# Kernel tuning notes

Hardware: AMD Instinct MI355X
Metric: run time of the kernel (lower is better)

## Reference

```python
import jax, jax.numpy as jnp
import numpy as np

N = 65536        # nodes = x_feature_num * batch_size
F_IN = 1024      # x_feature_num (conv1 in_channels)
E = 2097152      # edges (avg degree 32)
B = 64           # batch_size (final Linear out_features)


def gcn_conv(x, src, dst, ew, W, b, n):
    """PyG GCNConv: linear -> sym-normalized scatter-add with self-loops (fill=1)."""
    h = x @ W                                              # [n, out]
    deg = jnp.zeros((n,), x.dtype).at[dst].add(ew) + 1.0   # in-degree incl. self-loop weight 1
    dinv = jax.lax.rsqrt(deg)                              # deg >= 1, no inf
    norm = dinv[src] * ew * dinv[dst]                      # [E]
    agg = jnp.zeros_like(h).at[dst].add(h[src] * norm[:, None])
    agg = agg + h * (dinv * dinv)[:, None]                 # self-loop messages
    return agg + b


def setup_inputs() -> dict:
    key = jax.random.key(0)
    ks = jax.random.split(key, 12)
    x = jax.random.normal(ks[0], (N, F_IN), dtype=jnp.float32)
    A = jax.random.randint(ks[1], (2, E), 0, N, dtype=jnp.int32)
    A_weights = jax.random.uniform(ks[2], (E,), dtype=jnp.float32)
    s = 0.05
    W1 = jax.random.normal(ks[3], (F_IN, 16), dtype=jnp.float32) * s
    b1 = jnp.zeros((16,), jnp.float32)
    W2 = jax.random.normal(ks[4], (16, 4), dtype=jnp.float32) * s
    b2 = jnp.zeros((4,), jnp.float32)
    W3 = jax.random.normal(ks[5], (4, 1), dtype=jnp.float32) * s
    b3 = jnp.zeros((1,), jnp.float32)
    W_out = jax.random.normal(ks[6], (B, N), dtype=jnp.float32) * (1.0 / np.sqrt(N))
    b_out = jnp.zeros((B,), jnp.float32)
    return {"x": x, "A": A, "A_weights": A_weights,
            "W1": W1, "b1": b1, "W2": W2, "b2": b2, "W3": W3, "b3": b3,
            "W_out": W_out, "b_out": b_out}


def reference(x, A, A_weights, W1, b1, W2, b2, W3, b3, W_out, b_out):
    src, dst = A[0], A[1]
    n = x.shape[0]
    h = jax.nn.relu(gcn_conv(x, src, dst, A_weights, W1, b1, n))
    # F.dropout is identity in eval mode
    h = jax.nn.relu(gcn_conv(h, src, dst, A_weights, W2, b2, n))
    h = jax.nn.relu(gcn_conv(h, src, dst, A_weights, W3, b3, n))
    flat = h.reshape(-1)                                   # [N]
    return flat @ W_out.T + b_out                          # [B]
```

## Files before the change

### kernel.cpp

```cpp
#include <hip/hip_runtime.h>

#define NNODES 65536
#define FIN 1024
#define NEDGES 2097152
#define NB 64
#define G 256
#define CH (NEDGES / G)
#define CAPR 96
#define CAPB 9216
#define SCAP 10240
#define RS 1284
#define WS 272

union GSMem {
  struct { float sx[4 * RS]; float sw[4 * WS]; } a;
  float red[256 * 16];
};

__global__ __launch_bounds__(256) void kgemmF(const float* __restrict__ x, const float* __restrict__ W1,
                                              float* __restrict__ h1) {
  __shared__ GSMem sm;
  const int t = threadIdx.x;
  const int jg = t & 3, ks = (t >> 2) & 3, rg = t >> 4;
  const int row0 = blockIdx.x * 64;
  float4 acc[4];
#pragma unroll
  for (int ri = 0; ri < 4; ++ri) acc[ri] = make_float4(0.f, 0.f, 0.f, 0.f);
  for (int ch = 0; ch < 16; ++ch) {
    const int c0 = ch * 64;
#pragma unroll
    for (int i = 0; i < 4; ++i) {
      const int v = t + i * 256;
      const int rr = v >> 4, kq = v & 15;
      *(float4*)&sm.a.sx[(kq >> 2) * RS + rr * 20 + (kq & 3) * 4] =
          *(const float4*)(x + (size_t)(row0 + rr) * FIN + c0 + kq * 4);
    }
    {
      const int kr = t >> 2, c4 = t & 3;
      *(float4*)&sm.a.sw[(kr >> 4) * WS + (kr & 15) * 16 + c4 * 4] =
          *(const float4*)(W1 + (size_t)(c0 + kr) * 16 + c4 * 4);
    }
    __syncthreads();
    const int xb = ks * RS + rg * 80;
    const int wb = ks * WS + jg * 4;
#pragma unroll
    for (int k4 = 0; k4 < 4; ++k4) {
      float4 w4[4];
#pragma unroll
      for (int kq = 0; kq < 4; ++kq) w4[kq] = *(const float4*)&sm.a.sw[wb + (k4 * 4 + kq) * 16];
#pragma unroll
      for (int ri = 0; ri < 4; ++ri) {
        const float4 x4 = *(const float4*)&sm.a.sx[xb + ri * 20 + k4 * 4];
        acc[ri].x = fmaf(x4.x, w4[0].x, fmaf(x4.y, w4[1].x, fmaf(x4.z, w4[2].x, fmaf(x4.w, w4[3].x, acc[ri].x))));
        acc[ri].y = fmaf(x4.x, w4[0].y, fmaf(x4.y, w4[1].y, fmaf(x4.z, w4[2].y, fmaf(x4.w, w4[3].y, acc[ri].y))));
        acc[ri].z = fmaf(x4.x, w4[0].z, fmaf(x4.y, w4[1].z, fmaf(x4.z, w4[2].z, fmaf(x4.w, w4[3].z, acc[ri].z))));
        acc[ri].w = fmaf(x4.x, w4[0].w, fmaf(x4.y, w4[1].w, fmaf(x4.z, w4[2].w, fmaf(x4.w, w4[3].w, acc[ri].w))));
      }
    }
    __syncthreads();
  }
#pragma unroll
  for (int ri = 0; ri < 4; ++ri) *(float4*)&sm.red[t * 16 + ri * 4] = acc[ri];
  __syncthreads();
  if (ks == 0) {
#pragma unroll
    for (int ri = 0; ri < 4; ++ri) {
      float4 s = acc[ri];
      const float4 a1 = *(const float4*)&sm.red[(t + 4) * 16 + ri * 4];
      const float4 a2 = *(const float4*)&sm.red[(t + 8) * 16 + ri * 4];
      const float4 a3 = *(const float4*)&sm.red[(t + 12) * 16 + ri * 4];
      s.x += a1.x + a2.x + a3.x;
      s.y += a1.y + a2.y + a3.y;
      s.z += a1.z + a2.z + a3.z;
      s.w += a1.w + a2.w + a3.w;
      *(float4*)(h1 + (size_t)(row0 + rg * 4 + ri) * 16 + jg * 4) = s;
    }
  }
}

__global__ __launch_bounds__(512) void kscatF(const int* __restrict__ src, const int* __restrict__ dst,
                                              const float* __restrict__ ew, int2* __restrict__ tmp,
                                              int* __restrict__ counts) {
  __shared__ int2 ent[CH];
  __shared__ int hist[256], excl[256], cursor[256], sh[256];
  const int t = threadIdx.x, blk = blockIdx.x;
  const int base = blk * CH;
  if (t < 256) hist[t] = 0;
  __syncthreads();
  int sa[16], da[16]; float wa[16];
#pragma unroll
  for (int i = 0; i < 16; ++i) {
    const int e = base + t + i * 512;
    sa[i] = src[e]; da[i] = dst[e]; wa[i] = ew[e];
    atomicAdd(&hist[((unsigned)da[i]) >> 8], 1);
  }
  __syncthreads();
  if (t < 256) sh[t] = hist[t];
  __syncthreads();
#pragma unroll
  for (int off = 1; off < 256; off <<= 1) {
    int a = (t < 256 && t >= off) ? sh[t - off] : 0;
    __syncthreads();
    if (t < 256) sh[t] += a;
    __syncthreads();
  }
  if (t < 256) {
    const int e = sh[t] - hist[t];
    excl[t] = e;
    cursor[t] = e;
    counts[t * 256 + blk] = hist[t];
  }
  __syncthreads();
#pragma unroll
  for (int i = 0; i < 16; ++i) {
    const int b = ((unsigned)da[i]) >> 8;
    const int pos = atomicAdd(&cursor[b], 1);
    ent[pos] = make_int2((sa[i] & 0xFFFF) | ((da[i] & 255) << 16) | (b << 24),
                         __float_as_int(wa[i]));
  }
  __syncthreads();
#pragma unroll
  for (int i = 0; i < 16; ++i) {
    const int idx = t + i * 512;
    const int2 p = ent[idx];
    const int b = ((unsigned)p.x) >> 24;
    const int local = idx - excl[b];
    if (local < CAPR)
      tmp[(size_t)(b * 256 + blk) * CAPR + local] = make_int2(p.x & 0x00FFFFFF, p.y);
  }
}

__global__ __launch_bounds__(512) void ksortE(const int2* __restrict__ tmp, const int* __restrict__ counts,
                                              int2* __restrict__ csr, int* __restrict__ rs,
                                              int* __restrict__ cnt, float* __restrict__ dinv,
                                              float* __restrict__ h1) {
  __shared__ int2 stg[SCAP];
  __shared__ int hist[256], excl[256], cursor[256];
  __shared__ float degacc[256], dloc[256];
  const int t = threadIdx.x, b = blockIdx.x;
  const int seg = t >> 1, half = t & 1;
  const int len = counts[b * 256 + seg];
  const size_t cellbase = (size_t)(b * 256 + seg) * CAPR;
  if (t < 256) { hist[t] = 0; degacc[t] = 0.f; }
  __syncthreads();
  for (int i = half; i < len; i += 2) {
    const int2 p = tmp[cellbase + i];
    const int fine = (p.x >> 16) & 255;
    atomicAdd(&hist[fine], 1);
    atomicAdd(&degacc[fine], __int_as_float(p.y));
  }
  __syncthreads();
  if (t < 256) excl[t] = hist[t];
  __syncthreads();
#pragma unroll
  for (int off = 1; off < 256; off <<= 1) {
    int a = (t < 256 && t >= off) ? excl[t - off] : 0;
    __syncthreads();
    if (t < 256) excl[t] += a;
    __syncthreads();
  }
  if (t < 256) {
    const int e = excl[t] - hist[t];
    cursor[t] = e;
    rs[b * 256 + t] = b * CAPB + e;
    cnt[b * 256 + t] = hist[t];
    const float dn = rsqrtf(1.0f + degacc[t]);
    dloc[t] = dn;
    dinv[b * 256 + t] = dn;
  }
  __syncthreads();
  for (int i = half; i < len; i += 2) {
    const int2 p = tmp[cellbase + i];
    const int fine = (p.x >> 16) & 255;
    const int pos = atomicAdd(&cursor[fine], 1);
    const int2 rec = make_int2(p.x & 0xFFFF, p.y);
    if (pos < SCAP) stg[pos] = rec;
    else csr[(size_t)b * CAPB + pos] = rec;
  }
  __syncthreads();
  const int ntot = excl[255];
  for (int j = t; j < ntot; j += 512) csr[(size_t)b * CAPB + j] = stg[j];
  for (int v = t; v < 1024; v += 512) {
    const int node = v >> 2, q = v & 3;
    float* hp = h1 + (size_t)(b * 256 + node) * 16 + q * 4;
    float4 h = *(float4*)hp;
    const float dn = dloc[node];
    h.x *= dn; h.y *= dn; h.z *= dn; h.w *= dn;
    *(float4*)hp = h;
  }
}

__global__ __launch_bounds__(256) void kgather1(const float* __restrict__ H1, const int* __restrict__ rs,
                                                const int* __restrict__ cnt, const int2* __restrict__ csr,
                                                const float* __restrict__ dinv,
                                                const float* __restrict__ W2, const float* __restrict__ b1,
                                                float* __restrict__ H2) {
  __shared__ float sh_t[4][16];
  const int tid = threadIdx.x, wv = tid >> 6, l = tid & 63;
  const int n = blockIdx.x * 4 + wv;
  const int f2 = l & 7, slot = l >> 3;
  const int beg = rs[n], len = cnt[n];
  float2 acc = make_float2(0.f, 0.f);
  int2 pcur;
  if (slot < len) pcur = csr[beg + slot];
  for (int j = slot; j < len; j += 8) {
    const int jn = j + 8;
    int2 pnext;
    if (jn < len) pnext = csr[beg + jn];
    const float w = __int_as_float(pcur.y);
    const float2 hv = *(const float2*)(H1 + (size_t)pcur.x * 16 + f2 * 2);
    acc.x = fmaf(w, hv.x, acc.x);
    acc.y = fmaf(w, hv.y, acc.y);
    pcur = pnext;
  }
  acc.x += __shfl_xor(acc.x, 8, 64);  acc.y += __shfl_xor(acc.y, 8, 64);
  acc.x += __shfl_xor(acc.x, 16, 64); acc.y += __shfl_xor(acc.y, 16, 64);
  acc.x += __shfl_xor(acc.x, 32, 64); acc.y += __shfl_xor(acc.y, 32, 64);
  if (slot == 0) {
    const float dn = dinv[n];
    const float2 hs = *(const float2*)(H1 + (size_t)n * 16 + f2 * 2);
    float t0 = dn * (acc.x + hs.x) + b1[f2 * 2];
    float t1 = dn * (acc.y + hs.y) + b1[f2 * 2 + 1];
    sh_t[wv][f2 * 2] = t0 > 0.f ? t0 : 0.f;
    sh_t[wv][f2 * 2 + 1] = t1 > 0.f ? t1 : 0.f;
  }
  __syncthreads();
  if (tid < 16) {
    const int w2 = tid >> 2, c = tid & 3;
    const int nn = blockIdx.x * 4 + w2;
    float s = 0.f;
#pragma unroll
    for (int ff = 0; ff < 16; ++ff) s = fmaf(sh_t[w2][ff], W2[ff * 4 + c], s);
    H2[(size_t)nn * 4 + c] = s * dinv[nn];
  }
}

__global__ __launch_bounds__(256) void kgather2(const float* __restrict__ H2, const int* __restrict__ rs,
                                                const int* __restrict__ cnt, const int2* __restrict__ csr,
                                                const float* __restrict__ dinv,
                                                const float* __restrict__ W3, const float* __restrict__ b2,
                                                float* __restrict__ H3) {
  const int tid = threadIdx.x, wv = tid >> 6, l = tid & 63;
  const int n = blockIdx.x * 4 + wv;
  const int f = l & 3, slot = l >> 2;
  const int beg = rs[n], len = cnt[n];
  float acc = 0.f;
  for (int j = slot; j < len; j += 16) {
    const int2 p = csr[beg + j];
    acc = fmaf(__int_as_float(p.y), H2[(size_t)p.x * 4 + f], acc);
  }
#pragma unroll
  for (int off = 4; off < 64; off <<= 1) acc += __shfl_xor(acc, off, 64);
  const float dn = dinv[n];
  float t = dn * (acc + H2[(size_t)n * 4 + f]) + b2[f];
  t = t > 0.f ? t : 0.f;
  float p = t * W3[f];
  p += __shfl_xor(p, 1, 64);
  p += __shfl_xor(p, 2, 64);
  if (l == 0) H3[n] = p * dn;
}

__global__ __launch_bounds__(256) void kgather3(const float* __restrict__ H3, const int* __restrict__ rs,
                                                const int* __restrict__ cnt, const int2* __restrict__ csr,
                                                const float* __restrict__ dinv,
                                                const float* __restrict__ b3, float* __restrict__ flat) {
  const int tid = threadIdx.x, wv = tid >> 6, l = tid & 63;
  const int n = blockIdx.x * 4 + wv;
  const int beg = rs[n], len = cnt[n];
  float acc = 0.f;
  for (int j = l; j < len; j += 64) {
    const int2 p = csr[beg + j];
    acc = fmaf(__int_as_float(p.y), H3[p.x], acc);
  }
#pragma unroll
  for (int off = 1; off < 64; off <<= 1) acc += __shfl_xor(acc, off, 64);
  if (l == 0) {
    const float dn = dinv[n];
    float t = dn * (acc + H3[n]) + b3[0];
    flat[n] = t > 0.f ? t : 0.f;
  }
}

__global__ __launch_bounds__(256) void kfinal(const float* __restrict__ flat, const float* __restrict__ Wout,
                                              float* __restrict__ part) {
  const int b = blockIdx.x >> 4, q = blockIdx.x & 15;
  const float4* __restrict__ f4 = (const float4*)(flat) + q * 1024;
  const float4* __restrict__ w4 = (const float4*)(Wout + (size_t)b * NNODES) + q * 1024;
  __shared__ float red[4];
  float s = 0.f;
  for (int i = threadIdx.x; i < 1024; i += 256) {
    const float4 a = f4[i];
    const float4 wv = w4[i];
    s += a.x * wv.x + a.y * wv.y + a.z * wv.z + a.w * wv.w;
  }
#pragma unroll
  for (int off = 32; off; off >>= 1) s += __shfl_down(s, off, 64);
  if ((threadIdx.x & 63) == 0) red[threadIdx.x >> 6] = s;
  __syncthreads();
  if (threadIdx.x == 0) part[blockIdx.x] = red[0] + red[1] + red[2] + red[3];
}

__global__ __launch_bounds__(64) void kfinsum(const float* __restrict__ part, const float* __restrict__ bout,
                                              float* __restrict__ out) {
  const int b = threadIdx.x;
  float s = bout[b];
#pragma unroll
  for (int q = 0; q < 16; ++q) s += part[b * 16 + q];
  out[b] = s;
}

extern "C" void kernel_launch(void* const* d_in, const int* in_sizes, int n_in,
                              void* d_out, int out_size, void* d_ws, size_t ws_size,
                              hipStream_t stream) {
  const float* x   = (const float*)d_in[0];
  const int*   A   = (const int*)d_in[1];
  const float* ew  = (const float*)d_in[2];
  const float* W1  = (const float*)d_in[3];
  const float* b1  = (const float*)d_in[4];
  const float* W2  = (const float*)d_in[5];
  const float* b2  = (const float*)d_in[6];
  const float* W3  = (const float*)d_in[7];
  const float* b3  = (const float*)d_in[8];
  const float* Wo  = (const float*)d_in[9];
  const float* bo  = (const float*)d_in[10];
  float* out = (float*)d_out;

  const int* src = A;
  const int* dst = A + NEDGES;

  char* p = (char*)d_ws;
  float* dinv   = (float*)p; p += sizeof(float) * NNODES;
  int*   rsofs  = (int*)p;   p += sizeof(int) * NNODES;
  int*   cnt    = (int*)p;   p += sizeof(int) * NNODES;
  int*   counts = (int*)p;   p += sizeof(int) * NNODES;
  float* part   = (float*)p; p += sizeof(float) * 1024;
  int2*  tmp    = (int2*)p;  p += sizeof(int2) * (size_t)NNODES * CAPR;
  int2*  csr    = (int2*)p;  p += sizeof(int2) * (size_t)G * CAPB;
  float* h1     = (float*)p; p += sizeof(float) * (size_t)NNODES * 16;
  float* H2     = (float*)p; p += sizeof(float) * (size_t)NNODES * 4;
  float* H3     = (float*)p; p += sizeof(float) * NNODES;
  float* flat   = (float*)p; p += sizeof(float) * NNODES;

  kgemmF<<<NNODES / 64, 256, 0, stream>>>(x, W1, h1);
  kscatF<<<G, 512, 0, stream>>>(src, dst, ew, tmp, counts);
  ksortE<<<G, 512, 0, stream>>>(tmp, counts, csr, rsofs, cnt, dinv, h1);
  kgather1<<<NNODES / 4, 256, 0, stream>>>(h1, rsofs, cnt, csr, dinv, W2, b1, H2);
  kgather2<<<NNODES / 4, 256, 0, stream>>>(H2, rsofs, cnt, csr, dinv, W3, b2, H3);
  kgather3<<<NNODES / 4, 256, 0, stream>>>(H3, rsofs, cnt, csr, dinv, b3, flat);
  kfinal<<<NB * 16, 256, 0, stream>>>(flat, Wo, part);
  kfinsum<<<1, 64, 0, stream>>>(part, bo, out);
}
```

Before: 219.3 us.

## Widen ksortE to 1024 threads, vectorize gather1 loads, drop final-sum kernel

ksortE now runs 1024 threads per block, with four threads per segment instead of two, to raise parallelism in the per-bucket histogram and scatter passes. kgather1 reads float4 feature slices and processes 16 edges per wavefront iteration instead of 8, which halves the number of loop trips per node. The kfinsum kernel is removed: kgather3 writes the output bias and kfinal atomically adds its partial sums into the output. This saves one launch, but the floating-point summation order of the final reduction becomes nondeterministic.

```diff
diff --git a/kernel.cpp b/kernel.cpp
--- a/kernel.cpp
+++ b/kernel.cpp
@@ -130,20 +130,20 @@
   }
 }
 
-__global__ __launch_bounds__(512) void ksortE(const int2* __restrict__ tmp, const int* __restrict__ counts,
-                                              int2* __restrict__ csr, int* __restrict__ rs,
-                                              int* __restrict__ cnt, float* __restrict__ dinv,
-                                              float* __restrict__ h1) {
+__global__ __launch_bounds__(1024) void ksortE(const int2* __restrict__ tmp, const int* __restrict__ counts,
+                                               int2* __restrict__ csr, int* __restrict__ rs,
+                                               int* __restrict__ cnt, float* __restrict__ dinv,
+                                               float* __restrict__ h1) {
   __shared__ int2 stg[SCAP];
   __shared__ int hist[256], excl[256], cursor[256];
   __shared__ float degacc[256], dloc[256];
   const int t = threadIdx.x, b = blockIdx.x;
-  const int seg = t >> 1, half = t & 1;
+  const int seg = t >> 2, q4 = t & 3;
   const int len = counts[b * 256 + seg];
   const size_t cellbase = (size_t)(b * 256 + seg) * CAPR;
   if (t < 256) { hist[t] = 0; degacc[t] = 0.f; }
   __syncthreads();
-  for (int i = half; i < len; i += 2) {
+  for (int i = q4; i < len; i += 4) {
     const int2 p = tmp[cellbase + i];
     const int fine = (p.x >> 16) & 255;
     atomicAdd(&hist[fine], 1);
@@ -169,7 +169,7 @@
     dinv[b * 256 + t] = dn;
   }
   __syncthreads();
-  for (int i = half; i < len; i += 2) {
+  for (int i = q4; i < len; i += 4) {
     const int2 p = tmp[cellbase + i];
     const int fine = (p.x >> 16) & 255;
     const int pos = atomicAdd(&cursor[fine], 1);
@@ -179,9 +179,9 @@
   }
   __syncthreads();
   const int ntot = excl[255];
-  for (int j = t; j < ntot; j += 512) csr[(size_t)b * CAPB + j] = stg[j];
-  for (int v = t; v < 1024; v += 512) {
-    const int node = v >> 2, q = v & 3;
+  for (int j = t; j < ntot; j += 1024) csr[(size_t)b * CAPB + j] = stg[j];
+  {
+    const int node = t >> 2, q = t & 3;
     float* hp = h1 + (size_t)(b * 256 + node) * 16 + q * 4;
     float4 h = *(float4*)hp;
     const float dn = dloc[node];
@@ -198,31 +198,41 @@
   __shared__ float sh_t[4][16];
   const int tid = threadIdx.x, wv = tid >> 6, l = tid & 63;
   const int n = blockIdx.x * 4 + wv;
-  const int f2 = l & 7, slot = l >> 3;
+  const int f4 = l & 3, slot = l >> 2;
   const int beg = rs[n], len = cnt[n];
-  float2 acc = make_float2(0.f, 0.f);
+  float4 acc = make_float4(0.f, 0.f, 0.f, 0.f);
   int2 pcur;
   if (slot < len) pcur = csr[beg + slot];
-  for (int j = slot; j < len; j += 8) {
-    const int jn = j + 8;
+  for (int j = slot; j < len; j += 16) {
+    const int jn = j + 16;
     int2 pnext;
     if (jn < len) pnext = csr[beg + jn];
     const float w = __int_as_float(pcur.y);
-    const float2 hv = *(const float2*)(H1 + (size_t)pcur.x * 16 + f2 * 2);
+    const float4 hv = *(const float4*)(H1 + (size_t)pcur.x * 16 + f4 * 4);
     acc.x = fmaf(w, hv.x, acc.x);
     acc.y = fmaf(w, hv.y, acc.y);
+    acc.z = fmaf(w, hv.z, acc.z);
+    acc.w = fmaf(w, hv.w, acc.w);
     pcur = pnext;
   }
-  acc.x += __shfl_xor(acc.x, 8, 64);  acc.y += __shfl_xor(acc.y, 8, 64);
-  acc.x += __shfl_xor(acc.x, 16, 64); acc.y += __shfl_xor(acc.y, 16, 64);
-  acc.x += __shfl_xor(acc.x, 32, 64); acc.y += __shfl_xor(acc.y, 32, 64);
+#pragma unroll
+  for (int off = 4; off < 64; off <<= 1) {
+    acc.x += __shfl_xor(acc.x, off, 64);
+    acc.y += __shfl_xor(acc.y, off, 64);
+    acc.z += __shfl_xor(acc.z, off, 64);
+    acc.w += __shfl_xor(acc.w, off, 64);
+  }
   if (slot == 0) {
     const float dn = dinv[n];
-    const float2 hs = *(const float2*)(H1 + (size_t)n * 16 + f2 * 2);
-    float t0 = dn * (acc.x + hs.x) + b1[f2 * 2];
-    float t1 = dn * (acc.y + hs.y) + b1[f2 * 2 + 1];
-    sh_t[wv][f2 * 2] = t0 > 0.f ? t0 : 0.f;
-    sh_t[wv][f2 * 2 + 1] = t1 > 0.f ? t1 : 0.f;
+    const float4 hs = *(const float4*)(H1 + (size_t)n * 16 + f4 * 4);
+    float t0 = dn * (acc.x + hs.x) + b1[f4 * 4 + 0];
+    float t1 = dn * (acc.y + hs.y) + b1[f4 * 4 + 1];
+    float t2 = dn * (acc.z + hs.z) + b1[f4 * 4 + 2];
+    float t3 = dn * (acc.w + hs.w) + b1[f4 * 4 + 3];
+    sh_t[wv][f4 * 4 + 0] = t0 > 0.f ? t0 : 0.f;
+    sh_t[wv][f4 * 4 + 1] = t1 > 0.f ? t1 : 0.f;
+    sh_t[wv][f4 * 4 + 2] = t2 > 0.f ? t2 : 0.f;
+    sh_t[wv][f4 * 4 + 3] = t3 > 0.f ? t3 : 0.f;
   }
   __syncthreads();
   if (tid < 16) {
@@ -263,8 +273,10 @@
 __global__ __launch_bounds__(256) void kgather3(const float* __restrict__ H3, const int* __restrict__ rs,
                                                 const int* __restrict__ cnt, const int2* __restrict__ csr,
                                                 const float* __restrict__ dinv,
-                                                const float* __restrict__ b3, float* __restrict__ flat) {
+                                                const float* __restrict__ b3, float* __restrict__ flat,
+                                                const float* __restrict__ bout, float* __restrict__ out) {
   const int tid = threadIdx.x, wv = tid >> 6, l = tid & 63;
+  if (blockIdx.x == 0 && tid < NB) out[tid] = bout[tid];
   const int n = blockIdx.x * 4 + wv;
   const int beg = rs[n], len = cnt[n];
   float acc = 0.f;
@@ -282,7 +294,7 @@
 }
 
 __global__ __launch_bounds__(256) void kfinal(const float* __restrict__ flat, const float* __restrict__ Wout,
-                                              float* __restrict__ part) {
+                                              float* __restrict__ out) {
   const int b = blockIdx.x >> 4, q = blockIdx.x & 15;
   const float4* __restrict__ f4 = (const float4*)(flat) + q * 1024;
   const float4* __restrict__ w4 = (const float4*)(Wout + (size_t)b * NNODES) + q * 1024;
@@ -297,16 +309,7 @@
   for (int off = 32; off; off >>= 1) s += __shfl_down(s, off, 64);
   if ((threadIdx.x & 63) == 0) red[threadIdx.x >> 6] = s;
   __syncthreads();
-  if (threadIdx.x == 0) part[blockIdx.x] = red[0] + red[1] + red[2] + red[3];
-}
-
-__global__ __launch_bounds__(64) void kfinsum(const float* __restrict__ part, const float* __restrict__ bout,
-                                              float* __restrict__ out) {
-  const int b = threadIdx.x;
-  float s = bout[b];
-#pragma unroll
-  for (int q = 0; q < 16; ++q) s += part[b * 16 + q];
-  out[b] = s;
+  if (threadIdx.x == 0) atomicAdd(&out[b], red[0] + red[1] + red[2] + red[3]);
 }
 
 extern "C" void kernel_launch(void* const* d_in, const int* in_sizes, int n_in,
@@ -333,7 +336,6 @@
   int*   rsofs  = (int*)p;   p += sizeof(int) * NNODES;
   int*   cnt    = (int*)p;   p += sizeof(int) * NNODES;
   int*   counts = (int*)p;   p += sizeof(int) * NNODES;
-  float* part   = (float*)p; p += sizeof(float) * 1024;
   int2*  tmp    = (int2*)p;  p += sizeof(int2) * (size_t)NNODES * CAPR;
   int2*  csr    = (int2*)p;  p += sizeof(int2) * (size_t)G * CAPB;
   float* h1     = (float*)p; p += sizeof(float) * (size_t)NNODES * 16;
@@ -343,10 +345,9 @@
 
   kgemmF<<<NNODES / 64, 256, 0, stream>>>(x, W1, h1);
   kscatF<<<G, 512, 0, stream>>>(src, dst, ew, tmp, counts);
-  ksortE<<<G, 512, 0, stream>>>(tmp, counts, csr, rsofs, cnt, dinv, h1);
+  ksortE<<<G, 1024, 0, stream>>>(tmp, counts, csr, rsofs, cnt, dinv, h1);
   kgather1<<<NNODES / 4, 256, 0, stream>>>(h1, rsofs, cnt, csr, dinv, W2, b1, H2);
   kgather2<<<NNODES / 4, 256, 0, stream>>>(H2, rsofs, cnt, csr, dinv, W3, b2, H3);
-  kgather3<<<NNODES / 4, 256, 0, stream>>>(H3, rsofs, cnt, csr, dinv, b3, flat);
-  kfinal<<<NB * 16, 256, 0, stream>>>(flat, Wo, part);
-  kfinsum<<<1, 64, 0, stream>>>(part, bo, out);
-}
+  kgather3<<<NNODES / 4, 256, 0, stream>>>(H3, rsofs, cnt, csr, dinv, b3, flat, bo, out);
+  kfinal<<<NB * 16, 256, 0, stream>>>(flat, Wo, out);
+}
```

New measurement: 209.1 us. 4.7% less time.
